# Performance work log

Hardware: AMD Instinct MI355X
Metric: run time of the kernel (lower is better)

The kernel has to match this reference:

```python
import jax, jax.numpy as jnp
import numpy as np

N, T, H, D = 32, 2048, 1024, 384

def setup_inputs() -> dict:
    key = jax.random.key(0)
    k1, k2, k3, k4, k5 = jax.random.split(key, 5)
    scale_h = 1.0 / np.sqrt(H)
    scale_d = 1.0 / np.sqrt(D)
    return {
        "gru_output": jax.random.normal(k1, (N, T, H), dtype=jnp.float32),
        "condition": jax.random.normal(k2, (N, D), dtype=jnp.float32),
        "W_h": jax.random.normal(k3, (H, H), dtype=jnp.float32) * scale_h,
        "W_c": jax.random.normal(k4, (D, H), dtype=jnp.float32) * scale_d,
        "bias": jnp.zeros((H,), dtype=jnp.float32),
        "v": jax.random.normal(k5, (H,), dtype=jnp.float32) * scale_h,
    }

def reference(gru_output, condition, W_h, W_c, bias, v):
    # h_proj: (N, T, H); c_proj: (N, 1, H)
    h_proj = jnp.einsum("nth,hk->ntk", gru_output, W_h)
    c_proj = jnp.einsum("nd,dk->nk", condition, W_c)[:, None, :]
    energy = jnp.tanh(h_proj + c_proj + bias)          # (N, T, H)
    scores = jnp.einsum("ntk,k->nt", energy, v)        # (N, T)
    weights = jax.nn.softmax(scores, axis=-1)          # (N, T)
    context = jnp.einsum("nth,nt->nh", gru_output, weights)  # (N, H)
    return context
```

## Files before the change

### kernel.cpp

```cpp
#include <hip/hip_runtime.h>
#include <hip/hip_bf16.h>

#define N_B 32
#define T_S 2048
#define H_D 1024
#define D_C 384
#define NT  (N_B * T_S)

typedef __attribute__((ext_vector_type(8))) short bf16x8;
typedef __attribute__((ext_vector_type(4))) float f32x4;

__device__ __forceinline__ ushort f2bf(float f) {
    union { float f; unsigned u; } x; x.f = f;
    unsigned u = x.u;
    unsigned r = (u + 0x7FFFu + ((u >> 16) & 1u)) >> 16;
    return (ushort)r;
}

__device__ __forceinline__ float bf2f(ushort u) {
    union { unsigned u; float f; } x; x.u = ((unsigned)u) << 16;
    return x.f;
}

__device__ __forceinline__ float fast_tanh(float x) {
    float e = __expf(2.0f * x);
    return 1.0f - 2.0f / (e + 1.0f);
}

__global__ __launch_bounds__(256) void convert_kernel(
    const float* __restrict__ g, ushort* __restrict__ gb)
{
    const size_t base = ((size_t)blockIdx.x * 256 + threadIdx.x) * 4;
    float4 v = *(const float4*)(g + base);
    ushort4 o;
    o.x = f2bf(v.x); o.y = f2bf(v.y); o.z = f2bf(v.z); o.w = f2bf(v.w);
    *(ushort4*)(gb + base) = o;
}

__global__ __launch_bounds__(256) void transpose_kernel(
    const float* __restrict__ W, ushort* __restrict__ Wt)
{
    __shared__ ushort tile[64 * 66];
    const int bx = blockIdx.x & 15;
    const int by = blockIdx.x >> 4;
    const int t = threadIdx.x;
    #pragma unroll
    for (int i = 0; i < 16; ++i) {
        int idx = t + i * 256;
        int r = idx >> 6, c = idx & 63;
        tile[r * 66 + c] = f2bf(W[(size_t)(by * 64 + r) * H_D + bx * 64 + c]);
    }
    __syncthreads();
    #pragma unroll
    for (int i = 0; i < 16; ++i) {
        int idx = t + i * 256;
        int r = idx >> 6, c = idx & 63;
        Wt[(size_t)(bx * 64 + r) * H_D + by * 64 + c] = tile[c * 66 + r];
    }
}

__global__ __launch_bounds__(256) void cproj_kernel(
    const float* __restrict__ cond, const float* __restrict__ Wc,
    const float* __restrict__ bias, float* __restrict__ cproj)
{
    const int idx = blockIdx.x * 256 + threadIdx.x;
    const int n = idx >> 10, k = idx & 1023;
    const int d0 = blockIdx.y * 96;
    float a0 = (blockIdx.y == 0) ? bias[k] : 0.f;
    float a1 = 0.f, a2 = 0.f, a3 = 0.f;
    const float* cp = cond + n * D_C;
    for (int d = d0; d < d0 + 96; d += 4) {
        a0 = fmaf(cp[d + 0], Wc[(size_t)(d + 0) * H_D + k], a0);
        a1 = fmaf(cp[d + 1], Wc[(size_t)(d + 1) * H_D + k], a1);
        a2 = fmaf(cp[d + 2], Wc[(size_t)(d + 2) * H_D + k], a2);
        a3 = fmaf(cp[d + 3], Wc[(size_t)(d + 3) * H_D + k], a3);
    }
    atomicAdd(&cproj[idx], (a0 + a1) + (a2 + a3));
}

#define BKq 32
#define TILE_U (256 * BKq)

__global__ __launch_bounds__(512, 2) void gemm5_kernel(
    const ushort* __restrict__ Ab, const ushort* __restrict__ Wt,
    const float* __restrict__ cproj, const float* __restrict__ v,
    float* __restrict__ spart)
{
    __shared__ __align__(16) ushort As[2][TILE_U];
    __shared__ __align__(16) ushort Bs[2][TILE_U];
    __shared__ float red[2][4][128];

    const int bid = blockIdx.x;
    const int wg  = (bid & 7) * 128 + (bid >> 3);
    const int mb  = wg >> 2;
    const int nb  = wg & 3;
    const int m0  = mb * 256;
    const int n0  = nb * 256;
    const int nbatch = mb >> 3;

    const int t = threadIdx.x;
    const int lane = t & 63;
    const int w = t >> 6;
    const int wm = w >> 2, wn = w & 3;
    const int ln = lane & 15, q = lane >> 4;
    const int csw = q ^ ((ln >> 1) & 3);

    const int srow = t >> 1;
    const int c0   = (t & 1) * 2;
    const int fsw  = (srow >> 1) & 3;
    const int wc0  = (c0 ^ fsw) * 8;
    const int wc1  = ((c0 + 1) ^ fsw) * 8;

    const ushort* aL = Ab + (size_t)(m0 + srow) * H_D + c0 * 8;
    const ushort* bL = Wt + (size_t)(n0 + srow) * H_D + c0 * 8;
    ushort* awp0 = (ushort*)As + srow * BKq + wc0;
    ushort* awp1 = (ushort*)As + srow * BKq + wc1;
    ushort* bwp0 = (ushort*)Bs + srow * BKq + wc0;
    ushort* bwp1 = (ushort*)Bs + srow * BKq + wc1;

    const ushort* aR = (const ushort*)As + (wm * 128 + ln) * BKq + csw * 8;
    const ushort* bR = (const ushort*)Bs + (wn * 64  + ln) * BKq + csw * 8;

    f32x4 acc[8][4];
    #pragma unroll
    for (int i = 0; i < 8; ++i)
        #pragma unroll
        for (int j = 0; j < 4; ++j)
            acc[i][j] = (f32x4){0.f, 0.f, 0.f, 0.f};

    bf16x8 sA0, sA1, sB0, sB1;

#define LOADS(kt) do { \
    const ushort* _a = aL + (kt) * BKq; \
    const ushort* _b = bL + (kt) * BKq; \
    sA0 = *(const bf16x8*)(_a);     sA1 = *(const bf16x8*)(_a + 8); \
    sB0 = *(const bf16x8*)(_b);     sB1 = *(const bf16x8*)(_b + 8); \
} while (0)

#define WRITES(buf) do { \
    *(bf16x8*)(awp0 + (buf) * TILE_U) = sA0; \
    *(bf16x8*)(awp1 + (buf) * TILE_U) = sA1; \
    *(bf16x8*)(bwp0 + (buf) * TILE_U) = sB0; \
    *(bf16x8*)(bwp1 + (buf) * TILE_U) = sB1; \
} while (0)

#define MF(i,j,A,B) acc[i][j] = __builtin_amdgcn_mfma_f32_16x16x32_bf16(A, B, acc[i][j], 0, 0, 0)

#define COMPUTE(RB) do { \
    const ushort* _ar = aR + (RB) * TILE_U; \
    const ushort* _br = bR + (RB) * TILE_U; \
    bf16x8 _b0 = *(const bf16x8*)(_br); \
    bf16x8 _b1 = *(const bf16x8*)(_br + 512); \
    bf16x8 _b2 = *(const bf16x8*)(_br + 1024); \
    bf16x8 _b3 = *(const bf16x8*)(_br + 1536); \
    bf16x8 _a0 = *(const bf16x8*)(_ar); \
    bf16x8 _a1 = *(const bf16x8*)(_ar + 512); \
    bf16x8 _a2 = *(const bf16x8*)(_ar + 1024); \
    bf16x8 _a3 = *(const bf16x8*)(_ar + 1536); \
    __builtin_amdgcn_s_setprio(1); \
    MF(0,0,_a0,_b0); MF(0,1,_a0,_b1); MF(0,2,_a0,_b2); MF(0,3,_a0,_b3); \
    MF(1,0,_a1,_b0); MF(1,1,_a1,_b1); MF(1,2,_a1,_b2); MF(1,3,_a1,_b3); \
    MF(2,0,_a2,_b0); MF(2,1,_a2,_b1); MF(2,2,_a2,_b2); MF(2,3,_a2,_b3); \
    MF(3,0,_a3,_b0); MF(3,1,_a3,_b1); MF(3,2,_a3,_b2); MF(3,3,_a3,_b3); \
    __builtin_amdgcn_s_setprio(0); \
    bf16x8 _a4 = *(const bf16x8*)(_ar + 2048); \
    bf16x8 _a5 = *(const bf16x8*)(_ar + 2560); \
    bf16x8 _a6 = *(const bf16x8*)(_ar + 3072); \
    bf16x8 _a7 = *(const bf16x8*)(_ar + 3584); \
    __builtin_amdgcn_s_setprio(1); \
    MF(4,0,_a4,_b0); MF(4,1,_a4,_b1); MF(4,2,_a4,_b2); MF(4,3,_a4,_b3); \
    MF(5,0,_a5,_b0); MF(5,1,_a5,_b1); MF(5,2,_a5,_b2); MF(5,3,_a5,_b3); \
    MF(6,0,_a6,_b0); MF(6,1,_a6,_b1); MF(6,2,_a6,_b2); MF(6,3,_a6,_b3); \
    MF(7,0,_a7,_b0); MF(7,1,_a7,_b1); MF(7,2,_a7,_b2); MF(7,3,_a7,_b3); \
    __builtin_amdgcn_s_setprio(0); \
} while (0)

#define FENCE do { \
    asm volatile("s_waitcnt lgkmcnt(0)" ::: "memory"); \
    __builtin_amdgcn_s_barrier(); \
    __builtin_amdgcn_sched_barrier(0); \
} while (0)

    LOADS(0);
    WRITES(0);
    LOADS(1);
    FENCE;

    #pragma unroll 1
    for (int kt = 0; kt < 30; kt += 2) {
        WRITES(1); LOADS(kt + 2); COMPUTE(0); FENCE;
        WRITES(0); LOADS(kt + 3); COMPUTE(1); FENCE;
    }
    WRITES(1); COMPUTE(0); FENCE;
    COMPUTE(1);

    float cpv[4], vv[4];
    {
        const float* cpn = cproj + (size_t)nbatch * H_D;
        #pragma unroll
        for (int j = 0; j < 4; ++j) {
            int col = n0 + wn * 64 + j * 16 + ln;
            cpv[j] = cpn[col];
            vv[j]  = v[col];
        }
    }
    #pragma unroll
    for (int i = 0; i < 8; ++i) {
        float s0 = 0.f, s1 = 0.f, s2 = 0.f, s3 = 0.f;
        #pragma unroll
        for (int j = 0; j < 4; ++j) {
            s0 += fast_tanh(acc[i][j][0] + cpv[j]) * vv[j];
            s1 += fast_tanh(acc[i][j][1] + cpv[j]) * vv[j];
            s2 += fast_tanh(acc[i][j][2] + cpv[j]) * vv[j];
            s3 += fast_tanh(acc[i][j][3] + cpv[j]) * vv[j];
        }
        #pragma unroll
        for (int off = 1; off < 16; off <<= 1) {
            s0 += __shfl_xor(s0, off);
            s1 += __shfl_xor(s1, off);
            s2 += __shfl_xor(s2, off);
            s3 += __shfl_xor(s3, off);
        }
        if (ln == 0) {
            red[wm][wn][i * 16 + q * 4 + 0] = s0;
            red[wm][wn][i * 16 + q * 4 + 1] = s1;
            red[wm][wn][i * 16 + q * 4 + 2] = s2;
            red[wm][wn][i * 16 + q * 4 + 3] = s3;
        }
    }
    __syncthreads();
    if (t < 256) {
        const int wm2 = t >> 7, row = t & 127;
        float val = red[wm2][0][row] + red[wm2][1][row]
                  + red[wm2][2][row] + red[wm2][3][row];
        spart[(size_t)nb * NT + m0 + wm2 * 128 + row] = val;
    }
}

__global__ __launch_bounds__(1024) void softmax8_kernel(
    const float* __restrict__ spart, float* __restrict__ weights)
{
    const int n = blockIdx.x;
    const int t = threadIdx.x;
    __shared__ float red[1024];
    float s0 = 0.f, s1 = 0.f;
    #pragma unroll
    for (int kb = 0; kb < 4; ++kb) {
        s0 += spart[(size_t)kb * NT + n * T_S + t];
        s1 += spart[(size_t)kb * NT + n * T_S + 1024 + t];
    }
    red[t] = fmaxf(s0, s1); __syncthreads();
    for (int s = 512; s > 0; s >>= 1) {
        if (t < s) red[t] = fmaxf(red[t], red[t + s]);
        __syncthreads();
    }
    const float mx = red[0];
    __syncthreads();
    float e0 = __expf(s0 - mx), e1 = __expf(s1 - mx);
    red[t] = e0 + e1; __syncthreads();
    for (int s = 512; s > 0; s >>= 1) {
        if (t < s) red[t] += red[t + s];
        __syncthreads();
    }
    const float inv = 1.0f / red[0];
    weights[n * T_S + t] = e0 * inv;
    weights[n * T_S + 1024 + t] = e1 * inv;
}

__global__ __launch_bounds__(256) void context3_kernel(
    const ushort* __restrict__ Ab, const float* __restrict__ weights,
    float* __restrict__ cpart)
{
    const int tb = blockIdx.x;
    const int n  = blockIdx.y;
    const int t  = threadIdx.x;
    float a0 = 0.f, a1 = 0.f, a2 = 0.f, a3 = 0.f;
    const float* wp = weights + n * T_S + tb * 128;
    const ushort* gp = Ab + (size_t)(n * T_S + tb * 128) * H_D + t * 4;
    #pragma unroll 8
    for (int tt = 0; tt < 128; ++tt) {
        float w = wp[tt];
        ushort4 gv = *(const ushort4*)(gp + (size_t)tt * H_D);
        a0 = fmaf(w, bf2f(gv.x), a0);
        a1 = fmaf(w, bf2f(gv.y), a1);
        a2 = fmaf(w, bf2f(gv.z), a2);
        a3 = fmaf(w, bf2f(gv.w), a3);
    }
    *(float4*)(cpart + ((size_t)tb * N_B + n) * H_D + t * 4) =
        make_float4(a0, a1, a2, a3);
}

__global__ __launch_bounds__(256) void reduce_kernel(
    const float* __restrict__ cpart, float* __restrict__ out)
{
    const int idx = blockIdx.x * 256 + threadIdx.x;
    float s = 0.f;
    #pragma unroll
    for (int tb = 0; tb < 16; ++tb)
        s += cpart[(size_t)tb * (N_B * H_D) + idx];
    out[idx] = s;
}

extern "C" void kernel_launch(void* const* d_in, const int* in_sizes, int n_in,
                              void* d_out, int out_size, void* d_ws, size_t ws_size,
                              hipStream_t stream)
{
    const float* gru  = (const float*)d_in[0];
    const float* cond = (const float*)d_in[1];
    const float* W_h  = (const float*)d_in[2];
    const float* W_c  = (const float*)d_in[3];
    const float* bias = (const float*)d_in[4];
    const float* v    = (const float*)d_in[5];
    float* out = (float*)d_out;

    char* ws = (char*)d_ws;
    const size_t szAb    = (size_t)NT * H_D * 2;
    const size_t szWt    = (size_t)H_D * H_D * 2;
    const size_t szCproj = (size_t)N_B * H_D * 4;
    const size_t szSpart = (size_t)8 * NT * 4;

    ushort* Ab    = (ushort*)ws;
    ushort* Wt    = (ushort*)(ws + szAb);
    float* cproj  = (float*)(ws + szAb + szWt);
    float* spart  = (float*)(ws + szAb + szWt + szCproj);
    float* cpart  = spart;
    float* wts    = (float*)(ws + szAb + szWt + szCproj + szSpart);

    hipMemsetAsync(cproj, 0, szCproj, stream);
    convert_kernel<<<65536, 256, 0, stream>>>(gru, Ab);
    transpose_kernel<<<256, 256, 0, stream>>>(W_h, Wt);
    cproj_kernel<<<dim3(128, 4), 256, 0, stream>>>(cond, W_c, bias, cproj);
    gemm5_kernel<<<1024, 512, 0, stream>>>(Ab, Wt, cproj, v, spart);
    softmax8_kernel<<<N_B, 1024, 0, stream>>>(spart, wts);
    context3_kernel<<<dim3(16, N_B), 256, 0, stream>>>(Ab, wts, cpart);
    reduce_kernel<<<128, 256, 0, stream>>>(cpart, out);
}
```

Before: 571.5 us.

## Fuse fp32-to-bf16 conversion into GEMM loads and read fp32 in context

Removes the standalone conversion kernel that wrote a bf16 copy of the GRU output. The GEMM now loads fp32 activations and packs them to bf16 with v_cvt_pk_bf16_f32 before writing to LDS. The context kernel reads the fp32 input directly. This saves a full read-write pass over the large activation tensor, at the cost of doubled global A traffic in the GEMM, more registers for the staged loads, and a larger read in the context kernel.

```diff
diff --git a/kernel.cpp b/kernel.cpp
--- a/kernel.cpp
+++ b/kernel.cpp
@@ -17,24 +17,15 @@
     return (ushort)r;
 }
 
-__device__ __forceinline__ float bf2f(ushort u) {
-    union { unsigned u; float f; } x; x.u = ((unsigned)u) << 16;
-    return x.f;
+__device__ __forceinline__ unsigned cvt2(float lo, float hi) {
+    unsigned r;
+    asm("v_cvt_pk_bf16_f32 %0, %1, %2" : "=v"(r) : "v"(lo), "v"(hi));
+    return r;
 }
 
 __device__ __forceinline__ float fast_tanh(float x) {
     float e = __expf(2.0f * x);
     return 1.0f - 2.0f / (e + 1.0f);
-}
-
-__global__ __launch_bounds__(256) void convert_kernel(
-    const float* __restrict__ g, ushort* __restrict__ gb)
-{
-    const size_t base = ((size_t)blockIdx.x * 256 + threadIdx.x) * 4;
-    float4 v = *(const float4*)(g + base);
-    ushort4 o;
-    o.x = f2bf(v.x); o.y = f2bf(v.y); o.z = f2bf(v.z); o.w = f2bf(v.w);
-    *(ushort4*)(gb + base) = o;
 }
 
 __global__ __launch_bounds__(256) void transpose_kernel(
@@ -81,8 +72,8 @@
 #define BKq 32
 #define TILE_U (256 * BKq)
 
-__global__ __launch_bounds__(512, 2) void gemm5_kernel(
-    const ushort* __restrict__ Ab, const ushort* __restrict__ Wt,
+__global__ __launch_bounds__(512, 2) void gemm6_kernel(
+    const float* __restrict__ gru, const ushort* __restrict__ Wt,
     const float* __restrict__ cproj, const float* __restrict__ v,
     float* __restrict__ spart)
 {
@@ -111,8 +102,8 @@
     const int wc0  = (c0 ^ fsw) * 8;
     const int wc1  = ((c0 + 1) ^ fsw) * 8;
 
-    const ushort* aL = Ab + (size_t)(m0 + srow) * H_D + c0 * 8;
-    const ushort* bL = Wt + (size_t)(n0 + srow) * H_D + c0 * 8;
+    const float*  aLf = gru + (size_t)(m0 + srow) * H_D + c0 * 8;
+    const ushort* bL  = Wt  + (size_t)(n0 + srow) * H_D + c0 * 8;
     ushort* awp0 = (ushort*)As + srow * BKq + wc0;
     ushort* awp1 = (ushort*)As + srow * BKq + wc1;
     ushort* bwp0 = (ushort*)Bs + srow * BKq + wc0;
@@ -128,18 +119,28 @@
         for (int j = 0; j < 4; ++j)
             acc[i][j] = (f32x4){0.f, 0.f, 0.f, 0.f};
 
-    bf16x8 sA0, sA1, sB0, sB1;
+    float4 fA0, fA1, fA2, fA3;
+    bf16x8 sB0, sB1;
 
 #define LOADS(kt) do { \
-    const ushort* _a = aL + (kt) * BKq; \
-    const ushort* _b = bL + (kt) * BKq; \
-    sA0 = *(const bf16x8*)(_a);     sA1 = *(const bf16x8*)(_a + 8); \
-    sB0 = *(const bf16x8*)(_b);     sB1 = *(const bf16x8*)(_b + 8); \
+    const float*  _a = aLf + (kt) * BKq; \
+    const ushort* _b = bL  + (kt) * BKq; \
+    fA0 = *(const float4*)(_a); \
+    fA1 = *(const float4*)(_a + 4); \
+    fA2 = *(const float4*)(_a + 8); \
+    fA3 = *(const float4*)(_a + 12); \
+    sB0 = *(const bf16x8*)(_b); \
+    sB1 = *(const bf16x8*)(_b + 8); \
 } while (0)
 
 #define WRITES(buf) do { \
-    *(bf16x8*)(awp0 + (buf) * TILE_U) = sA0; \
-    *(bf16x8*)(awp1 + (buf) * TILE_U) = sA1; \
+    uint4 _w0, _w1; \
+    _w0.x = cvt2(fA0.x, fA0.y); _w0.y = cvt2(fA0.z, fA0.w); \
+    _w0.z = cvt2(fA1.x, fA1.y); _w0.w = cvt2(fA1.z, fA1.w); \
+    _w1.x = cvt2(fA2.x, fA2.y); _w1.y = cvt2(fA2.z, fA2.w); \
+    _w1.z = cvt2(fA3.x, fA3.y); _w1.w = cvt2(fA3.z, fA3.w); \
+    *(uint4*)(awp0 + (buf) * TILE_U) = _w0; \
+    *(uint4*)(awp1 + (buf) * TILE_U) = _w1; \
     *(bf16x8*)(bwp0 + (buf) * TILE_U) = sB0; \
     *(bf16x8*)(bwp1 + (buf) * TILE_U) = sB1; \
 } while (0)
@@ -267,8 +268,8 @@
     weights[n * T_S + 1024 + t] = e1 * inv;
 }
 
-__global__ __launch_bounds__(256) void context3_kernel(
-    const ushort* __restrict__ Ab, const float* __restrict__ weights,
+__global__ __launch_bounds__(256) void context4_kernel(
+    const float* __restrict__ gru, const float* __restrict__ weights,
     float* __restrict__ cpart)
 {
     const int tb = blockIdx.x;
@@ -276,15 +277,15 @@
     const int t  = threadIdx.x;
     float a0 = 0.f, a1 = 0.f, a2 = 0.f, a3 = 0.f;
     const float* wp = weights + n * T_S + tb * 128;
-    const ushort* gp = Ab + (size_t)(n * T_S + tb * 128) * H_D + t * 4;
+    const float* gp = gru + (size_t)(n * T_S + tb * 128) * H_D + t * 4;
     #pragma unroll 8
     for (int tt = 0; tt < 128; ++tt) {
-        float w = wp[tt];
-        ushort4 gv = *(const ushort4*)(gp + (size_t)tt * H_D);
-        a0 = fmaf(w, bf2f(gv.x), a0);
-        a1 = fmaf(w, bf2f(gv.y), a1);
-        a2 = fmaf(w, bf2f(gv.z), a2);
-        a3 = fmaf(w, bf2f(gv.w), a3);
+        float wv = wp[tt];
+        float4 gv = *(const float4*)(gp + (size_t)tt * H_D);
+        a0 = fmaf(wv, gv.x, a0);
+        a1 = fmaf(wv, gv.y, a1);
+        a2 = fmaf(wv, gv.z, a2);
+        a3 = fmaf(wv, gv.w, a3);
     }
     *(float4*)(cpart + ((size_t)tb * N_B + n) * H_D + t * 4) =
         make_float4(a0, a1, a2, a3);
@@ -319,7 +320,6 @@
     const size_t szCproj = (size_t)N_B * H_D * 4;
     const size_t szSpart = (size_t)8 * NT * 4;
 
-    ushort* Ab    = (ushort*)ws;
     ushort* Wt    = (ushort*)(ws + szAb);
     float* cproj  = (float*)(ws + szAb + szWt);
     float* spart  = (float*)(ws + szAb + szWt + szCproj);
@@ -327,11 +327,10 @@
     float* wts    = (float*)(ws + szAb + szWt + szCproj + szSpart);
 
     hipMemsetAsync(cproj, 0, szCproj, stream);
-    convert_kernel<<<65536, 256, 0, stream>>>(gru, Ab);
     transpose_kernel<<<256, 256, 0, stream>>>(W_h, Wt);
     cproj_kernel<<<dim3(128, 4), 256, 0, stream>>>(cond, W_c, bias, cproj);
-    gemm5_kernel<<<1024, 512, 0, stream>>>(Ab, Wt, cproj, v, spart);
+    gemm6_kernel<<<1024, 512, 0, stream>>>(gru, Wt, cproj, v, spart);
     softmax8_kernel<<<N_B, 1024, 0, stream>>>(spart, wts);
-    context3_kernel<<<dim3(16, N_B), 256, 0, stream>>>(Ab, wts, cpart);
+    context4_kernel<<<dim3(16, N_B), 256, 0, stream>>>(gru, wts, cpart);
     reduce_kernel<<<128, 256, 0, stream>>>(cpart, out);
 }
```

New measurement: 586.1 us. 2.5% more time.
